# Kernel optimization log

Measured on AMD Instinct MI355X. Metric: run time of the kernel, lower is better.

## Reference

```python
import jax, jax.numpy as jnp
import numpy as np

N = 10_000_000   # number of input events
SIZE = 2000      # output vector length (input-code vocabulary)

def setup_inputs() -> dict:
    key = jax.random.key(0)
    k_idx, k_rate, k_start, k_dur = jax.random.split(key, 4)
    index = jax.random.randint(k_idx, (N,), 0, SIZE, dtype=jnp.int32)
    rate = jax.random.uniform(k_rate, (N,), dtype=jnp.float32)
    starttime = jax.random.uniform(k_start, (N,), dtype=jnp.float32) * 100.0
    duration = jax.random.uniform(k_dur, (N,), dtype=jnp.float32) * 10.0
    endtime = starttime + duration
    t = jnp.float32(50.0)
    return {"index": index, "rate": rate, "starttime": starttime,
            "endtime": endtime, "t": t, "size": SIZE}

def reference(index, rate, starttime, endtime, t, size):
    # mask = events active at time t; gather rates of active events;
    # scatter-add into a fixed-size vector.
    # Faithful jit-friendly form: instead of boolean-gathering (data-dependent
    # shape), zero out inactive rates and scatter-add all events -- identical math.
    mask = (starttime <= t) & (t < endtime)
    contrib = jnp.where(mask, rate, jnp.zeros((), rate.dtype))
    adm_input = jnp.zeros((size,), dtype=rate.dtype)
    return adm_input.at[index].add(contrib)
```

## Files before the change

### kernel.cpp

```cpp
#include <hip/hip_runtime.h>


#define MAX_BINS 2048
#define HIST_BLOCK 1024

__global__ void __launch_bounds__(HIST_BLOCK)
hist_partial_kernel(const int* __restrict__ index,
                    const float* __restrict__ rate,
                    const float* __restrict__ starttime,
                    const float* __restrict__ endtime,
                    const float* __restrict__ t_ptr,
                    float* __restrict__ ws,
                    float* __restrict__ out,
                    int n, int size)
{
    __shared__ float hist[MAX_BINS];
    for (int j = threadIdx.x; j < size; j += blockDim.x) hist[j] = 0.0f;

    if (blockIdx.x == 0) {
        for (int j = threadIdx.x; j < size; j += blockDim.x) out[j] = 0.0f;
    }
    __syncthreads();

    const float t = t_ptr[0];
    const int tid      = blockIdx.x * blockDim.x + threadIdx.x;
    const int nthreads = gridDim.x * blockDim.x;
    const int nvec     = n >> 2;

    const int4*   idx4v = reinterpret_cast<const int4*>(index);
    const float4* rat4v = reinterpret_cast<const float4*>(rate);
    const float4* st4v  = reinterpret_cast<const float4*>(starttime);
    const float4* en4v  = reinterpret_cast<const float4*>(endtime);

    int i = tid;

    for (; i + nthreads < nvec; i += 2 * nthreads) {
        const int ib = i + nthreads;

        const float4 sA = st4v[i];  const float4 eA = en4v[i];
        const int4   iA = idx4v[i]; const float4 rA = rat4v[i];
        const float4 sB = st4v[ib];  const float4 eB = en4v[ib];
        const int4   iB = idx4v[ib]; const float4 rB = rat4v[ib];

        if ((sA.x <= t) & (t < eA.x)) atomicAdd(&hist[iA.x], rA.x);
        if ((sA.y <= t) & (t < eA.y)) atomicAdd(&hist[iA.y], rA.y);
        if ((sA.z <= t) & (t < eA.z)) atomicAdd(&hist[iA.z], rA.z);
        if ((sA.w <= t) & (t < eA.w)) atomicAdd(&hist[iA.w], rA.w);

        if ((sB.x <= t) & (t < eB.x)) atomicAdd(&hist[iB.x], rB.x);
        if ((sB.y <= t) & (t < eB.y)) atomicAdd(&hist[iB.y], rB.y);
        if ((sB.z <= t) & (t < eB.z)) atomicAdd(&hist[iB.z], rB.z);
        if ((sB.w <= t) & (t < eB.w)) atomicAdd(&hist[iB.w], rB.w);
    }

    for (; i < nvec; i += nthreads) {
        const float4 s4 = st4v[i];  const float4 e4 = en4v[i];
        const int4   i4 = idx4v[i]; const float4 r4 = rat4v[i];
        if ((s4.x <= t) & (t < e4.x)) atomicAdd(&hist[i4.x], r4.x);
        if ((s4.y <= t) & (t < e4.y)) atomicAdd(&hist[i4.y], r4.y);
        if ((s4.z <= t) & (t < e4.z)) atomicAdd(&hist[i4.z], r4.z);
        if ((s4.w <= t) & (t < e4.w)) atomicAdd(&hist[i4.w], r4.w);
    }

    for (int k = (nvec << 2) + tid; k < n; k += nthreads) {
        if (starttime[k] <= t && t < endtime[k]) atomicAdd(&hist[index[k]], rate[k]);
    }

    __syncthreads();

    float* part = ws + (size_t)blockIdx.x * size;
    const int nq = size >> 2;
    float4* part4 = reinterpret_cast<float4*>(part);
    const float4* hist4 = reinterpret_cast<const float4*>(hist);
    for (int j = threadIdx.x; j < nq; j += blockDim.x) part4[j] = hist4[j];
    for (int j = (nq << 2) + threadIdx.x; j < size; j += blockDim.x) part[j] = hist[j];
}

__global__ void __launch_bounds__(256)
reduce_partials_kernel(const float* __restrict__ ws,
                       float* __restrict__ out,
                       int npart, int size)
{
    const int j = blockIdx.x * blockDim.x + threadIdx.x;
    if (j >= size) return;

    const int chunk  = npart / gridDim.y;
    const int bstart = blockIdx.y * chunk;
    const int bend   = (blockIdx.y == gridDim.y - 1) ? npart : bstart + chunk;

    float sum = 0.0f;
    int b = bstart;
    #pragma unroll 8
    for (; b + 8 <= bend; b += 8) {
        sum += ws[(size_t)(b + 0) * size + j];
        sum += ws[(size_t)(b + 1) * size + j];
        sum += ws[(size_t)(b + 2) * size + j];
        sum += ws[(size_t)(b + 3) * size + j];
        sum += ws[(size_t)(b + 4) * size + j];
        sum += ws[(size_t)(b + 5) * size + j];
        sum += ws[(size_t)(b + 6) * size + j];
        sum += ws[(size_t)(b + 7) * size + j];
    }
    for (; b < bend; ++b) sum += ws[(size_t)b * size + j];

    atomicAdd(&out[j], sum);
}

__global__ void __launch_bounds__(256)
direct_atomic_kernel(const int* __restrict__ index,
                     const float* __restrict__ rate,
                     const float* __restrict__ starttime,
                     const float* __restrict__ endtime,
                     const float* __restrict__ t_ptr,
                     float* __restrict__ out, int n)
{
    const float t = t_ptr[0];
    const int tid      = blockIdx.x * blockDim.x + threadIdx.x;
    const int nthreads = gridDim.x * blockDim.x;
    for (int i = tid; i < n; i += nthreads) {
        if (starttime[i] <= t && t < endtime[i]) atomicAdd(&out[index[i]], rate[i]);
    }
}

extern "C" void kernel_launch(void* const* d_in, const int* in_sizes, int n_in,
                              void* d_out, int out_size, void* d_ws, size_t ws_size,
                              hipStream_t stream)
{
    const int*   index     = (const int*)  d_in[0];
    const float* rate      = (const float*)d_in[1];
    const float* starttime = (const float*)d_in[2];
    const float* endtime   = (const float*)d_in[3];
    const float* t_ptr     = (const float*)d_in[4];

    float* out = (float*)d_out;
    float* ws  = (float*)d_ws;
    const int n    = in_sizes[0];
    const int size = out_size;

    int npart = (int)(ws_size / ((size_t)size * sizeof(float)));
    if (npart > 256) npart = 256;

    if (size <= MAX_BINS && npart >= 64) {
        hist_partial_kernel<<<npart, HIST_BLOCK, 0, stream>>>(
            index, rate, starttime, endtime, t_ptr, ws, out, n, size);

        dim3 g2((size + 255) / 256, 16);
        reduce_partials_kernel<<<g2, 256, 0, stream>>>(ws, out, npart, size);
    } else {
        hipMemsetAsync(out, 0, (size_t)size * sizeof(float), stream);
        int grid = (n + 255) / 256;
        if (grid > 2048) grid = 2048;
        direct_atomic_kernel<<<grid, 256, 0, stream>>>(
            index, rate, starttime, endtime, t_ptr, out, n);
    }
}
```

Before: 31.48 us.

## Fuse histogram and partial reduction into one cooperative kernel with grid sync

Merges the per-block histogram kernel and the partial-sum reduction kernel into a single cooperative launch. Blocks sync across the grid after writing their partials, then each block reduces eight output bins across all 256 partials with shuffles and shared memory, writing the outputs directly instead of using atomics and a zeroing pass. This removes a second kernel launch and the atomic adds to the output, but adds a grid-wide barrier and a cooperative-launch requirement. The reduce kernel is simplified but no longer used on this path.

```diff
diff --git a/kernel.cpp b/kernel.cpp
--- a/kernel.cpp
+++ b/kernel.cpp
@@ -1,25 +1,26 @@
 #include <hip/hip_runtime.h>
+#include <hip/hip_cooperative_groups.h>
+
+namespace cg = cooperative_groups;
 
 
 #define MAX_BINS 2048
 #define HIST_BLOCK 1024
+#define NPART 256
+#define BPB 8
 
 __global__ void __launch_bounds__(HIST_BLOCK)
-hist_partial_kernel(const int* __restrict__ index,
-                    const float* __restrict__ rate,
-                    const float* __restrict__ starttime,
-                    const float* __restrict__ endtime,
-                    const float* __restrict__ t_ptr,
-                    float* __restrict__ ws,
-                    float* __restrict__ out,
-                    int n, int size)
+fused_hist_reduce_kernel(const int* __restrict__ index,
+                         const float* __restrict__ rate,
+                         const float* __restrict__ starttime,
+                         const float* __restrict__ endtime,
+                         const float* __restrict__ t_ptr,
+                         float* __restrict__ ws,
+                         float* __restrict__ out,
+                         int n, int size)
 {
     __shared__ float hist[MAX_BINS];
     for (int j = threadIdx.x; j < size; j += blockDim.x) hist[j] = 0.0f;
-
-    if (blockIdx.x == 0) {
-        for (int j = threadIdx.x; j < size; j += blockDim.x) out[j] = 0.0f;
-    }
     __syncthreads();
 
     const float t = t_ptr[0];
@@ -68,13 +69,45 @@
 
     __syncthreads();
 
-    float* part = ws + (size_t)blockIdx.x * size;
-    const int nq = size >> 2;
-    float4* part4 = reinterpret_cast<float4*>(part);
-    const float4* hist4 = reinterpret_cast<const float4*>(hist);
-    for (int j = threadIdx.x; j < nq; j += blockDim.x) part4[j] = hist4[j];
-    for (int j = (nq << 2) + threadIdx.x; j < size; j += blockDim.x) part[j] = hist[j];
+    {
+        float* part = ws + (size_t)blockIdx.x * size;
+        const int nq = size >> 2;
+        float4* part4 = reinterpret_cast<float4*>(part);
+        const float4* hist4 = reinterpret_cast<const float4*>(hist);
+        for (int j = threadIdx.x; j < nq; j += blockDim.x) part4[j] = hist4[j];
+        for (int j = (nq << 2) + threadIdx.x; j < size; j += blockDim.x) part[j] = hist[j];
+    }
+
+    cg::this_grid().sync();
+
+    const int j0 = blockIdx.x * BPB;
+    if (j0 < size) {
+        const int t2 = threadIdx.x;
+        const int jj = t2 & (BPB - 1);
+        const int h  = t2 >> 3;
+        const int j  = j0 + jj;
+
+        float s = 0.0f;
+        if (j < size) {
+            for (int p = h; p < NPART; p += (HIST_BLOCK >> 3))
+                s += ws[(size_t)p * size + j];
+        }
+        s += __shfl_down(s, 32);
+        s += __shfl_down(s, 16);
+        s += __shfl_down(s, 8);
+
+        if ((t2 & 63) < BPB) hist[(t2 >> 6) * BPB + jj] = s;
+        __syncthreads();
+        if (t2 < BPB) {
+            float tot = 0.0f;
+            #pragma unroll
+            for (int w = 0; w < (HIST_BLOCK / 64); ++w) tot += hist[w * BPB + t2];
+            const int j2 = j0 + t2;
+            if (j2 < size) out[j2] = tot;
+        }
+    }
 }
+
 
 __global__ void __launch_bounds__(256)
 reduce_partials_kernel(const float* __restrict__ ws,
@@ -83,26 +116,11 @@
 {
     const int j = blockIdx.x * blockDim.x + threadIdx.x;
     if (j >= size) return;
-
     const int chunk  = npart / gridDim.y;
     const int bstart = blockIdx.y * chunk;
     const int bend   = (blockIdx.y == gridDim.y - 1) ? npart : bstart + chunk;
-
     float sum = 0.0f;
-    int b = bstart;
-    #pragma unroll 8
-    for (; b + 8 <= bend; b += 8) {
-        sum += ws[(size_t)(b + 0) * size + j];
-        sum += ws[(size_t)(b + 1) * size + j];
-        sum += ws[(size_t)(b + 2) * size + j];
-        sum += ws[(size_t)(b + 3) * size + j];
-        sum += ws[(size_t)(b + 4) * size + j];
-        sum += ws[(size_t)(b + 5) * size + j];
-        sum += ws[(size_t)(b + 6) * size + j];
-        sum += ws[(size_t)(b + 7) * size + j];
-    }
-    for (; b < bend; ++b) sum += ws[(size_t)b * size + j];
-
+    for (int b = bstart; b < bend; ++b) sum += ws[(size_t)b * size + j];
     atomicAdd(&out[j], sum);
 }
 
@@ -134,18 +152,19 @@
 
     float* out = (float*)d_out;
     float* ws  = (float*)d_ws;
-    const int n    = in_sizes[0];
-    const int size = out_size;
+    int n    = in_sizes[0];
+    int size = out_size;
 
-    int npart = (int)(ws_size / ((size_t)size * sizeof(float)));
-    if (npart > 256) npart = 256;
+    const bool fused_ok = (size <= MAX_BINS) && (size <= NPART * BPB) &&
+                          (ws_size >= (size_t)NPART * (size_t)size * sizeof(float));
 
-    if (size <= MAX_BINS && npart >= 64) {
-        hist_partial_kernel<<<npart, HIST_BLOCK, 0, stream>>>(
-            index, rate, starttime, endtime, t_ptr, ws, out, n, size);
-
-        dim3 g2((size + 255) / 256, 16);
-        reduce_partials_kernel<<<g2, 256, 0, stream>>>(ws, out, npart, size);
+    if (fused_ok) {
+        void* args[] = { (void*)&index, (void*)&rate, (void*)&starttime,
+                         (void*)&endtime, (void*)&t_ptr, (void*)&ws,
+                         (void*)&out, (void*)&n, (void*)&size };
+        hipLaunchCooperativeKernel((void*)fused_hist_reduce_kernel,
+                                   dim3(NPART), dim3(HIST_BLOCK),
+                                   args, 0, stream);
     } else {
         hipMemsetAsync(out, 0, (size_t)size * sizeof(float), stream);
         int grid = (n + 255) / 256;
```

After: 76.74 us. +143.8%, slower.
